# Kernel optimization log

Hardware: AMD Instinct MI355X
Metric: run time of the kernel (lower is better)

The kernel has to match this reference:

```python
import jax, jax.numpy as jnp
import numpy as np

EPS = 1.1920929e-07  # torch nn.RMSNorm default eps = finfo(fp32).eps
H, NOPE, ROPE, VD = 16, 128, 64, 128
QKD = NOPE + ROPE


def rmsnorm(x, w):
    return x * jax.lax.rsqrt(jnp.mean(x * x, axis=-1, keepdims=True) + EPS) * w


def rope(x, cos, sin):
    # x: [B,S,h,D]; cos/sin broadcast to [B,S,h,D//2]; pairs are (even, odd) interleaved
    x2 = x.reshape(*x.shape[:-1], -1, 2)
    x0, x1 = x2[..., 0], x2[..., 1]
    r = x0 * cos - x1 * sin
    i = x0 * sin + x1 * cos
    return jnp.stack([r, i], axis=-1).reshape(x.shape)


def setup_inputs() -> dict:
    key = jax.random.key(0)
    ks = jax.random.split(key, 8)
    B, S, D = 2, 2048, 2048
    QR, KR = 1536, 512
    x = jax.random.normal(ks[0], (B, S, D), jnp.float32)
    # RoPE table: theta=10000, rope dim 64 -> 32 frequencies
    pos = np.arange(S)[:, None]
    inv = 1.0 / (10000.0 ** (np.arange(0, ROPE, 2) / ROPE))[None, :]
    ang = pos * inv
    freqs_cos = jnp.asarray(np.cos(ang), jnp.float32)
    freqs_sin = jnp.asarray(np.sin(ang), jnp.float32)

    def w(k, out_dim, in_dim):
        return jax.random.normal(k, (out_dim, in_dim), jnp.float32) / np.sqrt(in_dim)

    return {
        "x": x,
        "freqs_cos": freqs_cos,
        "freqs_sin": freqs_sin,
        "Wq_down": w(ks[1], QR, D),
        "q_norm_w": jnp.ones((QR,), jnp.float32),
        "Wq_up": w(ks[2], H * QKD, QR),
        "Wkv_down": w(ks[3], ROPE + KR, D),
        "kv_norm_w": jnp.ones((KR,), jnp.float32),
        "Wkv_up": w(ks[4], H * (VD + NOPE), KR),
        "Wo": w(ks[5], D, H * VD),
        "bo": jnp.zeros((D,), jnp.float32),
        "start_pos": 0,
    }


def reference(x, freqs_cos, freqs_sin, Wq_down, q_norm_w, Wq_up, Wkv_down, kv_norm_w, Wkv_up, Wo, bo, start_pos):
    B, S, D = x.shape
    cos = freqs_cos[None, :, None, :]
    sin = freqs_sin[None, :, None, :]
    # low-rank Q path: down -> RMSNorm -> up
    q = rmsnorm(x @ Wq_down.T, q_norm_w) @ Wq_up.T
    q = q.reshape(B, S, H, QKD)
    q_nope, q_rope = q[..., :NOPE], q[..., NOPE:]
    q_rope = rope(q_rope, cos, sin)
    q = jnp.concatenate([q_nope, q_rope], axis=-1)  # [B,S,H,QKD]
    # low-rank KV path: shared rope part + latent kv
    kv = x @ Wkv_down.T
    k_rope, c_kv = kv[..., :ROPE], kv[..., ROPE:]
    k_rope = rope(k_rope[:, :, None, :], cos, sin)  # [B,S,1,ROPE]
    kv = rmsnorm(c_kv, kv_norm_w) @ Wkv_up.T
    kv = kv.reshape(B, S, H, NOPE + VD)
    k_nope, v = kv[..., :NOPE], kv[..., NOPE:]
    k = jnp.concatenate([k_nope, jnp.broadcast_to(k_rope, (B, S, H, ROPE))], axis=-1)
    # causal SDPA (start_pos=0 prefill: cache slice equals fresh K/V)
    scale = 1.0 / np.sqrt(QKD)
    scores = jnp.einsum("bqhd,bkhd->bhqk", q, k) * scale
    mask = jnp.tril(jnp.ones((S, S), bool))
    scores = jnp.where(mask, scores, -jnp.inf)
    attn = jax.nn.softmax(scores, axis=-1)
    o = jnp.einsum("bhqk,bkhd->bqhd", attn, v).reshape(B, S, H * VD)
    return o @ Wo.T + bo
```

## Files before the change

### kernel.cpp

```cpp
#include <hip/hip_runtime.h>
#include <hip/hip_bf16.h>
#include <stdint.h>


typedef short bf16x8 __attribute__((ext_vector_type(8)));
typedef float f32x4  __attribute__((ext_vector_type(4)));
typedef unsigned int u32;

#define RMS_EPS 1.1920929e-07f
#define SCALE_L2E 0.10411931095f

__device__ __forceinline__ unsigned short f2b(float f) {
  union { float f; uint32_t u; } c; c.f = f;
  uint32_t u = c.u;
  return (unsigned short)((u + 0x7FFFu + ((u >> 16) & 1u)) >> 16);
}
__device__ __forceinline__ float b2f(short s) {
  union { uint32_t u; float f; } c; c.u = ((uint32_t)(unsigned short)s) << 16;
  return c.f;
}
__device__ __forceinline__ u32 pk2(float a, float b) {
  union { __hip_bfloat162 h; u32 u; } cv;
  cv.h = __float22bfloat162_rn(float2{a, b});
  return cv.u;
}
__device__ __forceinline__ void gld16(const short* g, short* l) {
  __builtin_amdgcn_global_load_lds(
      (const __attribute__((address_space(1))) u32*)g,
      (__attribute__((address_space(3))) u32*)l, 16, 0, 0);
}

__device__ __forceinline__ void cvt4(const float* __restrict__ in,
                                     short* __restrict__ out, int i) {
  float4 v = ((const float4*)in)[i];
  union { ushort4 s; uint2 u; } o;
  o.s.x = f2b(v.x); o.s.y = f2b(v.y); o.s.z = f2b(v.z); o.s.w = f2b(v.w);
  ((uint2*)out)[i] = o.u;
}

__global__ void f2bf_all_kernel(
    const float* __restrict__ x,    short* __restrict__ x_bf,
    const float* __restrict__ Wqd,  short* __restrict__ w_qd,
    const float* __restrict__ Wqu,  short* __restrict__ w_qu,
    const float* __restrict__ Wkvu, short* __restrict__ w_kvu,
    const float* __restrict__ Wo,   short* __restrict__ w_o,
    const float* __restrict__ Wkvd, short* __restrict__ w_kvd) {
  int i = blockIdx.x * 256 + threadIdx.x;
  if (i < 2097152) { cvt4(x, x_bf, i); return; }
  i -= 2097152;
  if (i < 786432) { cvt4(Wqd, w_qd, i); return; }
  i -= 786432;
  if (i < 1179648) { cvt4(Wqu, w_qu, i); return; }
  i -= 1179648;
  if (i < 524288) { cvt4(Wkvu, w_kvu, i); return; }
  i -= 524288;
  if (i < 1048576) { cvt4(Wo, w_o, i); return; }
  i -= 1048576;
  if (i >= 327680) return;
  int row = i >> 9;
  ushort4 s = {0, 0, 0, 0};
  if (row < 576) {
    float4 v = ((const float4*)Wkvd)[i];
    s.x = f2b(v.x); s.y = f2b(v.y); s.z = f2b(v.z); s.w = f2b(v.w);
  }
  union { ushort4 ss; uint2 u; } o; o.ss = s;
  ((uint2*)w_kvd)[i] = o.u;
}

template <int EPI>
__global__ __launch_bounds__(256) void gemm_bt(
    const short* __restrict__ A, const short* __restrict__ Bt,
    void* __restrict__ Cv, const float* __restrict__ bias,
    int K, int ldc,
    const float* __restrict__ fc, const float* __restrict__ fs,
    short* __restrict__ aux) {
  __shared__ __align__(16) short As[128 * 32];
  __shared__ __align__(16) short Bs[128 * 32];
  int nx = gridDim.x;
  int lin = blockIdx.y * nx + blockIdx.x;
  int cpx = (nx * gridDim.y) >> 3;
  int swz = (lin & 7) * cpx + (lin >> 3);
  int row0 = (swz / nx) * 128, col0 = (swz % nx) * 128;
  int t = threadIdx.x, lane = t & 63, w = t >> 6;
  int wm = w >> 1, wn = w & 1;
  int l15 = lane & 15, l4 = lane >> 4;
  f32x4 acc[4][4] = {};

  int srow = lane >> 2, scol = (lane & 3) * 8;
  const short* Ag = A + (size_t)(row0 + srow) * K + scol;
  const short* Bg = Bt + (size_t)(col0 + srow) * K + scol;

  for (int kt = 0; kt < K; kt += 32) {
#pragma unroll
    for (int c = 0; c < 2; ++c) {
      int blk = w * 2 + c;
      gld16(Ag + (size_t)(blk * 16) * K + kt, As + blk * 512);
      gld16(Bg + (size_t)(blk * 16) * K + kt, Bs + blk * 512);
    }
    __syncthreads();
    bf16x8 af[4], bfr[4];
#pragma unroll
    for (int i = 0; i < 4; ++i) {
      af[i]  = *(const bf16x8*)(As + (wm * 64 + i * 16 + l15) * 32 + l4 * 8);
      bfr[i] = *(const bf16x8*)(Bs + (wn * 64 + i * 16 + l15) * 32 + l4 * 8);
    }
#pragma unroll
    for (int i = 0; i < 4; ++i)
#pragma unroll
      for (int j = 0; j < 4; ++j)
        acc[i][j] = __builtin_amdgcn_mfma_f32_16x16x32_bf16(af[i], bfr[j], acc[i][j], 0, 0, 0);
    __syncthreads();
  }

  if constexpr (EPI == 0) {
    float* C = (float*)Cv;
#pragma unroll
    for (int j = 0; j < 4; ++j) {
      int col = col0 + wn * 64 + j * 16 + l15;
      float bv = bias ? bias[col] : 0.0f;
#pragma unroll
      for (int i = 0; i < 4; ++i) {
        int row = row0 + wm * 64 + i * 16 + l4 * 4;
        float* dst = C + (size_t)row * ldc + col;
#pragma unroll
        for (int r = 0; r < 4; ++r) dst[(size_t)r * ldc] = acc[i][j][r] + bv;
      }
    }
  } else if constexpr (EPI == 1) {
    short* C = (short*)Cv;
#pragma unroll
    for (int j = 0; j < 4; ++j) {
      int col = col0 + wn * 64 + j * 16 + l15;
#pragma unroll
      for (int i = 0; i < 4; ++i) {
        int row = row0 + wm * 64 + i * 16 + l4 * 4;
        short* dst = C + (size_t)row * ldc + col;
#pragma unroll
        for (int r = 0; r < 4; ++r) dst[(size_t)r * ldc] = (short)f2b(acc[i][j][r]);
      }
    }
  } else if constexpr (EPI == 2) {
    short* qb = (short*)Cv;
#pragma unroll
    for (int j = 0; j < 4; ++j) {
      int col = col0 + wn * 64 + j * 16 + l15;
      int h = col / 192;
      int d = col - h * 192;
      bool ro = (d >= 128);
      int ir = ro ? ((d - 128) >> 1) : 0;
      bool odd = (l15 & 1);
#pragma unroll
      for (int i = 0; i < 4; ++i) {
        int rowb = row0 + wm * 64 + i * 16 + l4 * 4;
#pragma unroll
        for (int r = 0; r < 4; ++r) {
          int row = rowb + r;
          int b = row >> 11, s = row & 2047;
          float v = acc[i][j][r];
          float pv = __shfl_xor(v, 1);
          float o;
          if (ro) {
            float c = fc[s * 32 + ir], sn = fs[s * 32 + ir];
            o = odd ? (pv * sn + v * c) : (v * c - pv * sn);
          } else {
            o = v;
          }
          qb[((size_t)((b * 16 + h) * 2048 + s)) * 192 + d] = (short)f2b(o * SCALE_L2E);
        }
      }
    }
  } else {
    short* kb = (short*)Cv;
    short* vT = aux;
    int h = col0 >> 8;
    if ((col0 & 128) == 0) {
#pragma unroll
      for (int j = 0; j < 4; ++j) {
        int d = wn * 64 + j * 16 + l15;
#pragma unroll
        for (int i = 0; i < 4; ++i) {
          int rowb = row0 + wm * 64 + i * 16 + l4 * 4;
#pragma unroll
          for (int r = 0; r < 4; ++r) {
            int row = rowb + r;
            int b = row >> 11, s = row & 2047;
            kb[((size_t)((b * 16 + h) * 2048 + s)) * 128 + d] = (short)f2b(acc[i][j][r]);
          }
        }
      }
    } else {
#pragma unroll
      for (int j = 0; j < 4; ++j) {
        int dv = wn * 64 + j * 16 + l15;
#pragma unroll
        for (int i = 0; i < 4; ++i) {
          int s0 = row0 + wm * 64 + i * 16 + l4 * 4;
          int b = s0 >> 11, s = s0 & 2047;
          short4 o;
          o.x = (short)f2b(acc[i][j][0]);
          o.y = (short)f2b(acc[i][j][1]);
          o.z = (short)f2b(acc[i][j][2]);
          o.w = (short)f2b(acc[i][j][3]);
          *(short4*)(vT + ((size_t)((b * 16 + h) * 128 + dv)) * 2048 + s) = o;
        }
      }
    }
  }
}

template <int W>
__global__ __launch_bounds__(256) void rmsnorm_wave(
    const short* __restrict__ in, const float* __restrict__ wgt,
    short* __restrict__ out, int ld_in) {
  constexpr int NC = W / 512;
  int row = blockIdx.x * 4 + (threadIdx.x >> 6);
  int lane = threadIdx.x & 63;
  const short* x = in + (size_t)row * ld_in + lane * 8;
  float vals[NC * 8];
  float ss = 0.f;
#pragma unroll
  for (int c = 0; c < NC; ++c) {
    bf16x8 v = *(const bf16x8*)(x + c * 512);
#pragma unroll
    for (int k = 0; k < 8; ++k) {
      float f = b2f(v[k]);
      vals[c * 8 + k] = f; ss += f * f;
    }
  }
#pragma unroll
  for (int off = 32; off > 0; off >>= 1) ss += __shfl_xor(ss, off);
  float rs = rsqrtf(ss / (float)W + RMS_EPS);
  short* o = out + (size_t)row * W + lane * 8;
#pragma unroll
  for (int c = 0; c < NC; ++c) {
    const float4* wp = (const float4*)(wgt + c * 512 + lane * 8);
    float4 w0 = wp[0], w1 = wp[1];
    ushort4 lo, hi;
    lo.x = f2b(vals[c * 8 + 0] * rs * w0.x);
    lo.y = f2b(vals[c * 8 + 1] * rs * w0.y);
    lo.z = f2b(vals[c * 8 + 2] * rs * w0.z);
    lo.w = f2b(vals[c * 8 + 3] * rs * w0.w);
    hi.x = f2b(vals[c * 8 + 4] * rs * w1.x);
    hi.y = f2b(vals[c * 8 + 5] * rs * w1.y);
    hi.z = f2b(vals[c * 8 + 6] * rs * w1.z);
    hi.w = f2b(vals[c * 8 + 7] * rs * w1.w);
    *(ushort4*)(o + c * 512) = lo;
    *(ushort4*)(o + c * 512 + 4) = hi;
  }
}

__global__ void prep_krope_kernel(const short* __restrict__ c1,
                                  const float* __restrict__ fc,
                                  const float* __restrict__ fs,
                                  short* __restrict__ kr) {
  int idx = blockIdx.x * 256 + threadIdx.x;
  int i = idx & 31;
  int s = (idx >> 5) & 2047;
  int b = idx >> 16;
  const short* row = c1 + (size_t)(b * 2048 + s) * 2176 + 1536 + 2 * i;
  float x0 = b2f(row[0]), x1 = b2f(row[1]);
  float c = fc[s * 32 + i], sn = fs[s * 32 + i];
  uint32_t pk = (uint32_t)f2b(x0 * c - x1 * sn) | ((uint32_t)f2b(x0 * sn + x1 * c) << 16);
  *(uint32_t*)(kr + ((size_t)(b * 2048 + s)) * 64 + 2 * i) = pk;
}

__global__ __launch_bounds__(256) void attn_kernel(
    const short* __restrict__ qb, const short* __restrict__ kb,
    const short* __restrict__ kr, const short* __restrict__ vtb,
    short* __restrict__ ob) {
  __shared__ __align__(16) short Ks[64 * 196];
  __shared__ __align__(16) short Vs[128 * 70];
  int bid = blockIdx.x;
  int xcd = bid & 7, rest = bid >> 3;
  int bh = xcd * 4 + (rest >> 5);
  int qt = 31 - (rest & 31);
  int b = bh >> 4, h = bh & 15;
  int t = threadIdx.x, lane = t & 63, w = t >> 6;
  int l15 = lane & 15, l4 = lane >> 4;
  const short* Kbh = kb + (size_t)bh * 2048 * 128;
  const short* krb = kr + (size_t)b * 2048 * 64;
  const short* Vbh = vtb + (size_t)bh * 128 * 2048;

  int sA = (l15 + ((l4 & 1) << 5)) << 2;
  int sB = sA + (16 << 2);
  bool chi = (l4 >> 1) != 0;

  int q0 = qt * 64;
  const short* Qbase = qb + ((size_t)bh * 2048 + q0 + w * 16) * 192;
  bf16x8 qf[6];
#pragma unroll
  for (int kk = 0; kk < 6; ++kk)
    qf[kk] = *(const bf16x8*)(Qbase + (size_t)l15 * 192 + kk * 32 + l4 * 8);
  f32x4 oaccT[8] = {};
  float m_i = -1e30f, l_i = 0.f;
  int qcol = q0 + w * 16 + l15;
  int kend = q0 + 64;

  for (int kt = 0; kt < kend; kt += 64) {
#pragma unroll
    for (int c = 0; c < 6; ++c) {
      int idx = t + 256 * c;
      int r = idx / 24, ch = idx - r * 24;
      const short* src = (ch < 16)
          ? Kbh + (size_t)(kt + r) * 128 + ch * 8
          : krb + (size_t)(kt + r) * 64 + (ch - 16) * 8;
      *(bf16x8*)(Ks + r * 196 + ch * 8) = *(const bf16x8*)src;
    }
#pragma unroll
    for (int c = 0; c < 4; ++c) {
      int idx = t + 256 * c;
      int d = idx >> 3, cc = (idx & 7) * 8;
      *(bf16x8*)(Vs + d * 70 + cc) =
          *(const bf16x8*)(Vbh + (size_t)d * 2048 + kt + cc);
    }
    __syncthreads();

    f32x4 s[4] = {};
    __builtin_amdgcn_s_setprio(1);
#pragma unroll
    for (int kk = 0; kk < 6; ++kk) {
#pragma unroll
      for (int c = 0; c < 4; ++c) {
        bf16x8 kf = *(const bf16x8*)(Ks + (c * 16 + l15) * 196 + kk * 32 + l4 * 8);
        s[c] = __builtin_amdgcn_mfma_f32_16x16x32_bf16(kf, qf[kk], s[c], 0, 0, 0);
      }
    }
    __builtin_amdgcn_s_setprio(0);

    if (kt == q0) {
#pragma unroll
      for (int c = 0; c < 4; ++c)
#pragma unroll
        for (int r = 0; r < 4; ++r) {
          int k = kt + c * 16 + l4 * 4 + r;
          if (k > qcol) s[c][r] = -1e30f;
        }
    }
    float mx = fmaxf(fmaxf(fmaxf(s[0][0], s[0][1]), fmaxf(s[0][2], s[0][3])),
                     fmaxf(fmaxf(s[1][0], s[1][1]), fmaxf(s[1][2], s[1][3])));
    mx = fmaxf(mx, fmaxf(fmaxf(fmaxf(s[2][0], s[2][1]), fmaxf(s[2][2], s[2][3])),
                         fmaxf(fmaxf(s[3][0], s[3][1]), fmaxf(s[3][2], s[3][3]))));
    mx = fmaxf(mx, __shfl_xor(mx, 16));
    mx = fmaxf(mx, __shfl_xor(mx, 32));
    float newm = fmaxf(m_i, mx);
    float alpha = __builtin_amdgcn_exp2f(m_i - newm);
    float rs = 0.f;
#pragma unroll
    for (int c = 0; c < 4; ++c)
#pragma unroll
      for (int r = 0; r < 4; ++r) {
        float p = __builtin_amdgcn_exp2f(s[c][r] - newm);
        s[c][r] = p; rs += p;
      }
    rs += __shfl_xor(rs, 16);
    rs += __shfl_xor(rs, 32);
    l_i = l_i * alpha + rs;
    m_i = newm;
#pragma unroll
    for (int dt = 0; dt < 8; ++dt)
#pragma unroll
      for (int r = 0; r < 4; ++r) oaccT[dt][r] *= alpha;

    u32 pk00 = pk2(s[0][0], s[0][1]), pk01 = pk2(s[0][2], s[0][3]);
    u32 pk10 = pk2(s[1][0], s[1][1]), pk11 = pk2(s[1][2], s[1][3]);
    u32 pk20 = pk2(s[2][0], s[2][1]), pk21 = pk2(s[2][2], s[2][3]);
    u32 pk30 = pk2(s[3][0], s[3][1]), pk31 = pk2(s[3][2], s[3][3]);
    union { bf16x8 v; u32 u[4]; } P0, P1;
    {
      u32 a0 = __builtin_amdgcn_ds_bpermute(sA, (int)pk00);
      u32 a1 = __builtin_amdgcn_ds_bpermute(sA, (int)pk01);
      u32 a2 = __builtin_amdgcn_ds_bpermute(sB, (int)pk00);
      u32 a3 = __builtin_amdgcn_ds_bpermute(sB, (int)pk01);
      u32 b0 = __builtin_amdgcn_ds_bpermute(sA, (int)pk10);
      u32 b1 = __builtin_amdgcn_ds_bpermute(sA, (int)pk11);
      u32 b2 = __builtin_amdgcn_ds_bpermute(sB, (int)pk10);
      u32 b3 = __builtin_amdgcn_ds_bpermute(sB, (int)pk11);
      P0.u[0] = chi ? b0 : a0; P0.u[1] = chi ? b1 : a1;
      P0.u[2] = chi ? b2 : a2; P0.u[3] = chi ? b3 : a3;
    }
    {
      u32 a0 = __builtin_amdgcn_ds_bpermute(sA, (int)pk20);
      u32 a1 = __builtin_amdgcn_ds_bpermute(sA, (int)pk21);
      u32 a2 = __builtin_amdgcn_ds_bpermute(sB, (int)pk20);
      u32 a3 = __builtin_amdgcn_ds_bpermute(sB, (int)pk21);
      u32 b0 = __builtin_amdgcn_ds_bpermute(sA, (int)pk30);
      u32 b1 = __builtin_amdgcn_ds_bpermute(sA, (int)pk31);
      u32 b2 = __builtin_amdgcn_ds_bpermute(sB, (int)pk30);
      u32 b3 = __builtin_amdgcn_ds_bpermute(sB, (int)pk31);
      P1.u[0] = chi ? b0 : a0; P1.u[1] = chi ? b1 : a1;
      P1.u[2] = chi ? b2 : a2; P1.u[3] = chi ? b3 : a3;
    }

    __builtin_amdgcn_s_setprio(1);
#pragma unroll
    for (int dt = 0; dt < 8; ++dt) {
      bf16x8 vf0 = *(const bf16x8*)(Vs + (dt * 16 + l15) * 70 + l4 * 8);
      bf16x8 vf1 = *(const bf16x8*)(Vs + (dt * 16 + l15) * 70 + 32 + l4 * 8);
      oaccT[dt] = __builtin_amdgcn_mfma_f32_16x16x32_bf16(vf0, P0.v, oaccT[dt], 0, 0, 0);
      oaccT[dt] = __builtin_amdgcn_mfma_f32_16x16x32_bf16(vf1, P1.v, oaccT[dt], 0, 0, 0);
    }
    __builtin_amdgcn_s_setprio(0);
    __syncthreads();
  }
  float inv = 1.0f / l_i;
  short* dst = ob + ((size_t)(b * 2048 + qcol)) * 2048 + h * 128;
#pragma unroll
  for (int dt = 0; dt < 8; ++dt) {
    uint2 o;
    o.x = pk2(oaccT[dt][0] * inv, oaccT[dt][1] * inv);
    o.y = pk2(oaccT[dt][2] * inv, oaccT[dt][3] * inv);
    *(uint2*)(dst + dt * 16 + l4 * 4) = o;
  }
}

extern "C" void kernel_launch(void* const* d_in, const int* in_sizes, int n_in,
                              void* d_out, int out_size, void* d_ws, size_t ws_size,
                              hipStream_t stream) {
  const float* x    = (const float*)d_in[0];
  const float* fcos = (const float*)d_in[1];
  const float* fsin = (const float*)d_in[2];
  const float* Wqd  = (const float*)d_in[3];
  const float* qnw  = (const float*)d_in[4];
  const float* Wqu  = (const float*)d_in[5];
  const float* Wkvd = (const float*)d_in[6];
  const float* kvnw = (const float*)d_in[7];
  const float* Wkvu = (const float*)d_in[8];
  const float* Wo   = (const float*)d_in[9];
  const float* bo   = (const float*)d_in[10];
  float* out = (float*)d_out;
  char* ws = (char*)d_ws;

  short* x_bf  = (short*)(ws + 0);
  short* w_cat = (short*)(ws + 16777216);
  short* w_qu  = (short*)(ws + 25690112);
  short* w_kvu = (short*)(ws + 35127296);
  short* w_o   = (short*)(ws + 39321600);
  short* c1    = (short*)(ws + 47710208);
  short* qn    = (short*)(ws + 65536000);
  short* ckvn  = (short*)(ws + 78118912);
  short* q_b   = (short*)(ws + 82313216);
  short* k_b   = (short*)(ws + 107479040);
  short* vT    = (short*)(ws + 132644864);
  short* o_bf  = (short*)(ws + 149422080);
  short* kr    = (short*)(ws + 166199296);

  f2bf_all_kernel<<<23296, 256, 0, stream>>>(x, x_bf, Wqd, w_cat, Wqu, w_qu,
                                             Wkvu, w_kvu, Wo, w_o,
                                             Wkvd, w_cat + 1536 * 2048);

  gemm_bt<1><<<dim3(17, 32), 256, 0, stream>>>(x_bf, w_cat, c1, nullptr, 2048, 2176,
                                               nullptr, nullptr, nullptr);
  prep_krope_kernel<<<512, 256, 0, stream>>>(c1, fcos, fsin, kr);
  rmsnorm_wave<1536><<<1024, 256, 0, stream>>>(c1, qnw, qn, 2176);
  rmsnorm_wave<512><<<1024, 256, 0, stream>>>(c1 + 1600, kvnw, ckvn, 2176);

  gemm_bt<2><<<dim3(24, 32), 256, 0, stream>>>(qn, w_qu, q_b, nullptr, 1536, 0,
                                               fcos, fsin, nullptr);
  gemm_bt<3><<<dim3(32, 32), 256, 0, stream>>>(ckvn, w_kvu, k_b, nullptr, 512, 0,
                                               nullptr, nullptr, vT);

  attn_kernel<<<1024, 256, 0, stream>>>(q_b, k_b, kr, vT, o_bf);

  gemm_bt<0><<<dim3(16, 32), 256, 0, stream>>>(o_bf, w_o, out, bo, 2048, 2048,
                                               nullptr, nullptr, nullptr);
}
```

Baseline: 389.9 us.

## Pair causal query tiles per attention block for balanced work

Each attention block now handles two query tiles, qx and 31-qx, in sequence, so every block does the same total amount of causal work, and the grid is halved to 512 blocks. The K/K-rope/V tile loads are also restructured into separate per-thread index patterns without the division by 24. The aim is to remove the tail imbalance of causal attention. The cost is fewer blocks in flight (512 on 256 CUs), less parallelism, and each block running longer serially.

```diff
diff --git a/kernel.cpp b/kernel.cpp
--- a/kernel.cpp
+++ b/kernel.cpp
@@ -271,9 +271,9 @@
   __shared__ __align__(16) short Ks[64 * 196];
   __shared__ __align__(16) short Vs[128 * 70];
   int bid = blockIdx.x;
-  int xcd = bid & 7, rest = bid >> 3;
-  int bh = xcd * 4 + (rest >> 5);
-  int qt = 31 - (rest & 31);
+  int xcd = bid & 7, kk2 = bid >> 3;
+  int bh = xcd * 4 + (kk2 >> 4);
+  int qx = kk2 & 15;
   int b = bh >> 4, h = bh & 15;
   int t = threadIdx.x, lane = t & 63, w = t >> 6;
   int l15 = lane & 15, l4 = lane >> 4;
@@ -281,135 +281,144 @@
   const short* krb = kr + (size_t)b * 2048 * 64;
   const short* Vbh = vtb + (size_t)bh * 128 * 2048;
 
+  int kn_r = t >> 4, kn_c = (t & 15) * 8;
+  int kr_r = t >> 3, kr_c = (t & 7) * 8;
+  int v_d = t >> 3, v_c = (t & 7) * 8;
+
   int sA = (l15 + ((l4 & 1) << 5)) << 2;
   int sB = sA + (16 << 2);
   bool chi = (l4 >> 1) != 0;
 
-  int q0 = qt * 64;
-  const short* Qbase = qb + ((size_t)bh * 2048 + q0 + w * 16) * 192;
-  bf16x8 qf[6];
-#pragma unroll
-  for (int kk = 0; kk < 6; ++kk)
-    qf[kk] = *(const bf16x8*)(Qbase + (size_t)l15 * 192 + kk * 32 + l4 * 8);
-  f32x4 oaccT[8] = {};
-  float m_i = -1e30f, l_i = 0.f;
-  int qcol = q0 + w * 16 + l15;
-  int kend = q0 + 64;
-
-  for (int kt = 0; kt < kend; kt += 64) {
-#pragma unroll
-    for (int c = 0; c < 6; ++c) {
-      int idx = t + 256 * c;
-      int r = idx / 24, ch = idx - r * 24;
-      const short* src = (ch < 16)
-          ? Kbh + (size_t)(kt + r) * 128 + ch * 8
-          : krb + (size_t)(kt + r) * 64 + (ch - 16) * 8;
-      *(bf16x8*)(Ks + r * 196 + ch * 8) = *(const bf16x8*)src;
-    }
-#pragma unroll
-    for (int c = 0; c < 4; ++c) {
-      int idx = t + 256 * c;
-      int d = idx >> 3, cc = (idx & 7) * 8;
-      *(bf16x8*)(Vs + d * 70 + cc) =
-          *(const bf16x8*)(Vbh + (size_t)d * 2048 + kt + cc);
-    }
-    __syncthreads();
-
-    f32x4 s[4] = {};
-    __builtin_amdgcn_s_setprio(1);
-#pragma unroll
-    for (int kk = 0; kk < 6; ++kk) {
+  for (int half = 0; half < 2; ++half) {
+    int qt = half ? (31 - qx) : qx;
+    int q0 = qt * 64;
+    const short* Qbase = qb + ((size_t)bh * 2048 + q0 + w * 16) * 192;
+    bf16x8 qf[6];
+#pragma unroll
+    for (int kk = 0; kk < 6; ++kk)
+      qf[kk] = *(const bf16x8*)(Qbase + (size_t)l15 * 192 + kk * 32 + l4 * 8);
+    f32x4 oaccT[8] = {};
+    float m_i = -1e30f, l_i = 0.f;
+    int qcol = q0 + w * 16 + l15;
+    int kend = q0 + 64;
+
+    for (int kt = 0; kt < kend; kt += 64) {
 #pragma unroll
       for (int c = 0; c < 4; ++c) {
-        bf16x8 kf = *(const bf16x8*)(Ks + (c * 16 + l15) * 196 + kk * 32 + l4 * 8);
-        s[c] = __builtin_amdgcn_mfma_f32_16x16x32_bf16(kf, qf[kk], s[c], 0, 0, 0);
-      }
-    }
-    __builtin_amdgcn_s_setprio(0);
-
-    if (kt == q0) {
+        int r = kn_r + 16 * c;
+        *(bf16x8*)(Ks + r * 196 + kn_c) =
+            *(const bf16x8*)(Kbh + (size_t)(kt + r) * 128 + kn_c);
+      }
+#pragma unroll
+      for (int c = 0; c < 2; ++c) {
+        int r = kr_r + 32 * c;
+        *(bf16x8*)(Ks + r * 196 + 128 + kr_c) =
+            *(const bf16x8*)(krb + (size_t)(kt + r) * 64 + kr_c);
+      }
+#pragma unroll
+      for (int c = 0; c < 4; ++c) {
+        int d = v_d + 32 * c;
+        *(bf16x8*)(Vs + d * 70 + v_c) =
+            *(const bf16x8*)(Vbh + (size_t)d * 2048 + kt + v_c);
+      }
+      __syncthreads();
+
+      f32x4 s[4] = {};
+      __builtin_amdgcn_s_setprio(1);
+#pragma unroll
+      for (int kk = 0; kk < 6; ++kk) {
+#pragma unroll
+        for (int c = 0; c < 4; ++c) {
+          bf16x8 kf = *(const bf16x8*)(Ks + (c * 16 + l15) * 196 + kk * 32 + l4 * 8);
+          s[c] = __builtin_amdgcn_mfma_f32_16x16x32_bf16(kf, qf[kk], s[c], 0, 0, 0);
+        }
+      }
+      __builtin_amdgcn_s_setprio(0);
+
+      if (kt == q0) {
+#pragma unroll
+        for (int c = 0; c < 4; ++c)
+#pragma unroll
+          for (int r = 0; r < 4; ++r) {
+            int k = kt + c * 16 + l4 * 4 + r;
+            if (k > qcol) s[c][r] = -1e30f;
+          }
+      }
+      float mx = fmaxf(fmaxf(fmaxf(s[0][0], s[0][1]), fmaxf(s[0][2], s[0][3])),
+                       fmaxf(fmaxf(s[1][0], s[1][1]), fmaxf(s[1][2], s[1][3])));
+      mx = fmaxf(mx, fmaxf(fmaxf(fmaxf(s[2][0], s[2][1]), fmaxf(s[2][2], s[2][3])),
+                           fmaxf(fmaxf(s[3][0], s[3][1]), fmaxf(s[3][2], s[3][3]))));
+      mx = fmaxf(mx, __shfl_xor(mx, 16));
+      mx = fmaxf(mx, __shfl_xor(mx, 32));
+      float newm = fmaxf(m_i, mx);
+      float alpha = __builtin_amdgcn_exp2f(m_i - newm);
+      float rs = 0.f;
 #pragma unroll
       for (int c = 0; c < 4; ++c)
 #pragma unroll
         for (int r = 0; r < 4; ++r) {
-          int k = kt + c * 16 + l4 * 4 + r;
-          if (k > qcol) s[c][r] = -1e30f;
+          float p = __builtin_amdgcn_exp2f(s[c][r] - newm);
+          s[c][r] = p; rs += p;
         }
-    }
-    float mx = fmaxf(fmaxf(fmaxf(s[0][0], s[0][1]), fmaxf(s[0][2], s[0][3])),
-                     fmaxf(fmaxf(s[1][0], s[1][1]), fmaxf(s[1][2], s[1][3])));
-    mx = fmaxf(mx, fmaxf(fmaxf(fmaxf(s[2][0], s[2][1]), fmaxf(s[2][2], s[2][3])),
-                         fmaxf(fmaxf(s[3][0], s[3][1]), fmaxf(s[3][2], s[3][3]))));
-    mx = fmaxf(mx, __shfl_xor(mx, 16));
-    mx = fmaxf(mx, __shfl_xor(mx, 32));
-    float newm = fmaxf(m_i, mx);
-    float alpha = __builtin_amdgcn_exp2f(m_i - newm);
-    float rs = 0.f;
-#pragma unroll
-    for (int c = 0; c < 4; ++c)
-#pragma unroll
-      for (int r = 0; r < 4; ++r) {
-        float p = __builtin_amdgcn_exp2f(s[c][r] - newm);
-        s[c][r] = p; rs += p;
-      }
-    rs += __shfl_xor(rs, 16);
-    rs += __shfl_xor(rs, 32);
-    l_i = l_i * alpha + rs;
-    m_i = newm;
-#pragma unroll
-    for (int dt = 0; dt < 8; ++dt)
-#pragma unroll
-      for (int r = 0; r < 4; ++r) oaccT[dt][r] *= alpha;
-
-    u32 pk00 = pk2(s[0][0], s[0][1]), pk01 = pk2(s[0][2], s[0][3]);
-    u32 pk10 = pk2(s[1][0], s[1][1]), pk11 = pk2(s[1][2], s[1][3]);
-    u32 pk20 = pk2(s[2][0], s[2][1]), pk21 = pk2(s[2][2], s[2][3]);
-    u32 pk30 = pk2(s[3][0], s[3][1]), pk31 = pk2(s[3][2], s[3][3]);
-    union { bf16x8 v; u32 u[4]; } P0, P1;
-    {
-      u32 a0 = __builtin_amdgcn_ds_bpermute(sA, (int)pk00);
-      u32 a1 = __builtin_amdgcn_ds_bpermute(sA, (int)pk01);
-      u32 a2 = __builtin_amdgcn_ds_bpermute(sB, (int)pk00);
-      u32 a3 = __builtin_amdgcn_ds_bpermute(sB, (int)pk01);
-      u32 b0 = __builtin_amdgcn_ds_bpermute(sA, (int)pk10);
-      u32 b1 = __builtin_amdgcn_ds_bpermute(sA, (int)pk11);
-      u32 b2 = __builtin_amdgcn_ds_bpermute(sB, (int)pk10);
-      u32 b3 = __builtin_amdgcn_ds_bpermute(sB, (int)pk11);
-      P0.u[0] = chi ? b0 : a0; P0.u[1] = chi ? b1 : a1;
-      P0.u[2] = chi ? b2 : a2; P0.u[3] = chi ? b3 : a3;
-    }
-    {
-      u32 a0 = __builtin_amdgcn_ds_bpermute(sA, (int)pk20);
-      u32 a1 = __builtin_amdgcn_ds_bpermute(sA, (int)pk21);
-      u32 a2 = __builtin_amdgcn_ds_bpermute(sB, (int)pk20);
-      u32 a3 = __builtin_amdgcn_ds_bpermute(sB, (int)pk21);
-      u32 b0 = __builtin_amdgcn_ds_bpermute(sA, (int)pk30);
-      u32 b1 = __builtin_amdgcn_ds_bpermute(sA, (int)pk31);
-      u32 b2 = __builtin_amdgcn_ds_bpermute(sB, (int)pk30);
-      u32 b3 = __builtin_amdgcn_ds_bpermute(sB, (int)pk31);
-      P1.u[0] = chi ? b0 : a0; P1.u[1] = chi ? b1 : a1;
-      P1.u[2] = chi ? b2 : a2; P1.u[3] = chi ? b3 : a3;
-    }
-
-    __builtin_amdgcn_s_setprio(1);
+      rs += __shfl_xor(rs, 16);
+      rs += __shfl_xor(rs, 32);
+      l_i = l_i * alpha + rs;
+      m_i = newm;
+#pragma unroll
+      for (int dt = 0; dt < 8; ++dt)
+#pragma unroll
+        for (int r = 0; r < 4; ++r) oaccT[dt][r] *= alpha;
+
+      u32 pk00 = pk2(s[0][0], s[0][1]), pk01 = pk2(s[0][2], s[0][3]);
+      u32 pk10 = pk2(s[1][0], s[1][1]), pk11 = pk2(s[1][2], s[1][3]);
+      u32 pk20 = pk2(s[2][0], s[2][1]), pk21 = pk2(s[2][2], s[2][3]);
+      u32 pk30 = pk2(s[3][0], s[3][1]), pk31 = pk2(s[3][2], s[3][3]);
+      union { bf16x8 v; u32 u[4]; } P0, P1;
+      {
+        u32 a0 = __builtin_amdgcn_ds_bpermute(sA, (int)pk00);
+        u32 a1 = __builtin_amdgcn_ds_bpermute(sA, (int)pk01);
+        u32 a2 = __builtin_amdgcn_ds_bpermute(sB, (int)pk00);
+        u32 a3 = __builtin_amdgcn_ds_bpermute(sB, (int)pk01);
+        u32 b0 = __builtin_amdgcn_ds_bpermute(sA, (int)pk10);
+        u32 b1 = __builtin_amdgcn_ds_bpermute(sA, (int)pk11);
+        u32 b2 = __builtin_amdgcn_ds_bpermute(sB, (int)pk10);
+        u32 b3 = __builtin_amdgcn_ds_bpermute(sB, (int)pk11);
+        P0.u[0] = chi ? b0 : a0; P0.u[1] = chi ? b1 : a1;
+        P0.u[2] = chi ? b2 : a2; P0.u[3] = chi ? b3 : a3;
+      }
+      {
+        u32 a0 = __builtin_amdgcn_ds_bpermute(sA, (int)pk20);
+        u32 a1 = __builtin_amdgcn_ds_bpermute(sA, (int)pk21);
+        u32 a2 = __builtin_amdgcn_ds_bpermute(sB, (int)pk20);
+        u32 a3 = __builtin_amdgcn_ds_bpermute(sB, (int)pk21);
+        u32 b0 = __builtin_amdgcn_ds_bpermute(sA, (int)pk30);
+        u32 b1 = __builtin_amdgcn_ds_bpermute(sA, (int)pk31);
+        u32 b2 = __builtin_amdgcn_ds_bpermute(sB, (int)pk30);
+        u32 b3 = __builtin_amdgcn_ds_bpermute(sB, (int)pk31);
+        P1.u[0] = chi ? b0 : a0; P1.u[1] = chi ? b1 : a1;
+        P1.u[2] = chi ? b2 : a2; P1.u[3] = chi ? b3 : a3;
+      }
+
+      __builtin_amdgcn_s_setprio(1);
+#pragma unroll
+      for (int dt = 0; dt < 8; ++dt) {
+        bf16x8 vf0 = *(const bf16x8*)(Vs + (dt * 16 + l15) * 70 + l4 * 8);
+        bf16x8 vf1 = *(const bf16x8*)(Vs + (dt * 16 + l15) * 70 + 32 + l4 * 8);
+        oaccT[dt] = __builtin_amdgcn_mfma_f32_16x16x32_bf16(vf0, P0.v, oaccT[dt], 0, 0, 0);
+        oaccT[dt] = __builtin_amdgcn_mfma_f32_16x16x32_bf16(vf1, P1.v, oaccT[dt], 0, 0, 0);
+      }
+      __builtin_amdgcn_s_setprio(0);
+      __syncthreads();
+    }
+    float inv = 1.0f / l_i;
+    short* dst = ob + ((size_t)(b * 2048 + qcol)) * 2048 + h * 128;
 #pragma unroll
     for (int dt = 0; dt < 8; ++dt) {
-      bf16x8 vf0 = *(const bf16x8*)(Vs + (dt * 16 + l15) * 70 + l4 * 8);
-      bf16x8 vf1 = *(const bf16x8*)(Vs + (dt * 16 + l15) * 70 + 32 + l4 * 8);
-      oaccT[dt] = __builtin_amdgcn_mfma_f32_16x16x32_bf16(vf0, P0.v, oaccT[dt], 0, 0, 0);
-      oaccT[dt] = __builtin_amdgcn_mfma_f32_16x16x32_bf16(vf1, P1.v, oaccT[dt], 0, 0, 0);
-    }
-    __builtin_amdgcn_s_setprio(0);
-    __syncthreads();
-  }
-  float inv = 1.0f / l_i;
-  short* dst = ob + ((size_t)(b * 2048 + qcol)) * 2048 + h * 128;
-#pragma unroll
-  for (int dt = 0; dt < 8; ++dt) {
-    uint2 o;
-    o.x = pk2(oaccT[dt][0] * inv, oaccT[dt][1] * inv);
-    o.y = pk2(oaccT[dt][2] * inv, oaccT[dt][3] * inv);
-    *(uint2*)(dst + dt * 16 + l4 * 4) = o;
+      uint2 o;
+      o.x = pk2(oaccT[dt][0] * inv, oaccT[dt][1] * inv);
+      o.y = pk2(oaccT[dt][2] * inv, oaccT[dt][3] * inv);
+      *(uint2*)(dst + dt * 16 + l4 * 4) = o;
+    }
   }
 }
 
@@ -459,7 +468,7 @@
   gemm_bt<3><<<dim3(32, 32), 256, 0, stream>>>(ckvn, w_kvu, k_b, nullptr, 512, 0,
                                                nullptr, nullptr, vT);
 
-  attn_kernel<<<1024, 256, 0, stream>>>(q_b, k_b, kr, vT, o_bf);
+  attn_kernel<<<512, 256, 0, stream>>>(q_b, k_b, kr, vT, o_bf);
 
   gemm_bt<0><<<dim3(16, 32), 256, 0, stream>>>(o_bf, w_o, out, bo, 2048, 2048,
                                                nullptr, nullptr, nullptr);
```

After: 354.4 us. 9.1% less time.
